# Kernel tuning notes

Measured on AMD Instinct MI355X. Metric: run time of the kernel, lower is better.

Reference implementation:

```python
import jax, jax.numpy as jnp
import numpy as np
import math

H = 1024
HEADS = 32
S = 4096
B = 3
E = 8192
QA = 2049  # start of QA span; content sentences cover [1, 2049)


def setup_inputs() -> dict:
    key = jax.random.key(0)
    ks = jax.random.split(key, 12)
    hidden_states = jax.random.normal(ks[0], (B, S, H), dtype=jnp.float32)
    st_mask = jax.random.randint(ks[1], (B, S), 0, 2, dtype=jnp.int64)
    edges_src = jax.random.randint(ks[2], (E,), 0, S, dtype=jnp.int64)
    edges_tgt = jax.random.randint(ks[3], (E,), 0, S, dtype=jnp.int64)
    edges_type = jax.random.randint(ks[4], (E,), 0, 26, dtype=jnp.int64)
    edges_pos = jax.random.randint(ks[5], (E,), 0, S, dtype=jnp.int64)
    # 32 content sentences of length 64 covering [1, 2049), then the QA span (2049, 4096)
    begins = 1 + 64 * np.arange(32)
    ends = begins + 64
    pairs = np.stack([np.append(begins, QA), np.append(ends, S)], axis=1).reshape(-1)
    all_sen = np.tile(pairs, (B, 1)).astype(np.int64)  # kept as numpy: static span indices
    scale = 0.02
    Wq = jax.random.normal(ks[6], (H, H), jnp.float32) * scale
    Wk = jax.random.normal(ks[7], (H, H), jnp.float32) * scale
    Wv = jax.random.normal(ks[8], (H, H), jnp.float32) * scale
    Wo = jax.random.normal(ks[9], (H, H), jnp.float32) * scale
    bq = jnp.zeros((H,), jnp.float32)
    bk = jnp.zeros((H,), jnp.float32)
    bv = jnp.zeros((H,), jnp.float32)
    bo = jnp.zeros((H,), jnp.float32)
    return dict(hidden_states=hidden_states, st_mask=st_mask, edges_src=edges_src,
                edges_tgt=edges_tgt, edges_type=edges_type, edges_pos=edges_pos,
                all_sen=all_sen, Wq=Wq, bq=bq, Wk=Wk, bk=bk, Wv=Wv, bv=bv, Wo=Wo, bo=bo)


def reference(hidden_states, st_mask, edges_src, edges_tgt, edges_type, edges_pos,
              all_sen, Wq, bq, Wk, bk, Wv, bv, Wo, bo):
    h = HEADS
    d_model = hidden_states.shape[-1]
    dk = d_model // h
    inv_sqrt_dk = 1.0 / math.sqrt(dk)

    def mha(q, k, v):
        # q: [Lq, H]; k, v: [Lk, H] -> [Lq, H]  (dropout is identity in eval mode)
        q2 = (q @ Wq.T + bq).reshape(-1, h, dk).transpose(1, 0, 2)  # [h, Lq, dk]
        k2 = (k @ Wk.T + bk).reshape(-1, h, dk).transpose(1, 0, 2)  # [h, Lk, dk]
        v2 = (v @ Wv.T + bv).reshape(-1, h, dk).transpose(1, 0, 2)
        scores = jnp.einsum('hqd,hkd->hqk', q2, k2) * inv_sqrt_dk
        p = jax.nn.softmax(scores, axis=-1)
        x = jnp.einsum('hqk,hkd->hqd', p, v2).transpose(1, 0, 2).reshape(-1, d_model)
        return x @ Wo.T + bo

    sen = np.asarray(all_sen)  # static span indices (host constants)
    outs = []
    for i in range(hidden_states.shape[0]):  # fixed small batch of 3
        pairs = sen[i][sen[i] != -1].reshape(-1, 2)
        qa, end = int(pairs[-1, 0]), int(pairs[-1, 1])
        q = hidden_states[i, 1:qa]       # [qa-1, H]
        kv = hidden_states[i, qa:end]    # [end-qa, H]
        hq1q2 = mha(q, kv, kv)           # content attends to QA span
        hq2q1 = mha(kv, q, q)            # QA span attends to content
        # hidden_states2 analogue: zeros elsewhere, attended reps in the two spans
        row = jnp.zeros_like(hidden_states[i])
        row = row.at[1:qa].set(hq1q2).at[qa:end].set(hq2q1)
        # per-sentence means (hidden_states3)
        sent_means = jnp.stack([row[b:e].mean(axis=0) for b, e in pairs])  # [n_sen, H]
        V11 = sent_means[:-1].mean(axis=0)  # mean over content-sentence means
        V21 = sent_means[-1]                # QA-span mean
        outs.append(jnp.concatenate([V11, V21]))
    return jnp.stack(outs)  # [3, 2H]
```

## Files before the change

### kernel.cpp

```cpp
#include <hip/hip_runtime.h>
#include <cstddef>

typedef __attribute__((ext_vector_type(8))) short bf16x8;
typedef __attribute__((ext_vector_type(4))) float f32x4;
typedef __attribute__((ext_vector_type(4))) unsigned short u16x4;
typedef __attribute__((ext_vector_type(8))) unsigned short u16x8;

namespace {
constexpr int B_ = 3, S_ = 4096, H_ = 1024, NH_ = 32;
constexpr int SEG1 = 1, SEG2 = 2049;
constexpr int NQ1 = 2048, NK1 = 2047, NQ2 = 2047, NK2 = 2048;
constexpr float SCALE = 0.17677669529663687f;
constexpr float LOG2E = 1.4426950408889634f;
constexpr float QSC   = SCALE * LOG2E;

constexpr size_t oXb = 0;
constexpr size_t oWb = oXb + (size_t)12288 * 1024 * 2;
constexpr size_t oBB = oWb + (size_t)2048 * 1024 * 2;
constexpr size_t oQH = oBB + (size_t)2048 * 4;
constexpr size_t oKH = oQH + (size_t)6 * 32 * 2048 * 32 * 2;
constexpr size_t oNL = oKH + (size_t)6 * 32 * 2048 * 32 * 2;
constexpr size_t oCS = oNL + (size_t)6 * 2048 * 4;
constexpr size_t oU  = oCS + (size_t)6 * 32 * 2048 * 4;
constexpr size_t oMv = oU  + (size_t)6 * 32 * 1024 * 4;
constexpr size_t oUP = oMv + (size_t)6 * 1024 * 4;
}

#if __has_builtin(__builtin_amdgcn_exp2f)
#define EXP2(x) __builtin_amdgcn_exp2f(x)
#else
#define EXP2(x) exp2f(x)
#endif
#if __has_builtin(__builtin_amdgcn_logf)
#define LOG2(x) __builtin_amdgcn_logf(x)
#else
#define LOG2(x) log2f(x)
#endif

__device__ __forceinline__ unsigned short f2bf(float f) {
    unsigned u = __float_as_uint(f);
    u += 0x7FFF + ((u >> 16) & 1);
    return (unsigned short)(u >> 16);
}
__device__ __forceinline__ float bf2f(unsigned short u) {
    return __uint_as_float((unsigned)u << 16);
}
__device__ __forceinline__ void gl16(const unsigned short* gp, unsigned short* lp) {
    __builtin_amdgcn_global_load_lds(
        (const __attribute__((address_space(1))) unsigned int*)gp,
        (__attribute__((address_space(3))) unsigned int*)lp, 16, 0, 0);
}

__global__ __launch_bounds__(256) void conv_x(const float* __restrict__ X,
                                              unsigned short* __restrict__ Xb)
{
    const size_t i4 = (size_t)blockIdx.x * 256 + threadIdx.x;
    const float4 v = *(const float4*)&X[i4 * 4];
    u16x4 o;
    o[0] = f2bf(v.x); o[1] = f2bf(v.y); o[2] = f2bf(v.z); o[3] = f2bf(v.w);
    *(u16x4*)&Xb[i4 * 4] = o;
}

__global__ __launch_bounds__(256) void conv_w(const float* __restrict__ Wq,
                                              const float* __restrict__ bq,
                                              const float* __restrict__ Wk,
                                              const float* __restrict__ bk,
                                              unsigned short* __restrict__ Wb,
                                              float* __restrict__ bb,
                                              unsigned short* __restrict__ QH,
                                              unsigned short* __restrict__ KH)
{
    const int i4 = blockIdx.x * 256 + threadIdx.x;
    const int base = i4 * 4;
    const bool isQ = base < (1 << 20);
    const float sc = isQ ? QSC : 1.f;
    const float* src = isQ ? &Wq[base] : &Wk[base - (1 << 20)];
    const float4 v = *(const float4*)src;
    u16x4 o;
    o[0] = f2bf(v.x * sc); o[1] = f2bf(v.y * sc);
    o[2] = f2bf(v.z * sc); o[3] = f2bf(v.w * sc);
    *(u16x4*)&Wb[base] = o;
    if (base < 2048) {
#pragma unroll
        for (int c = 0; c < 4; ++c) {
            const int j = base + c;
            bb[j] = (j < 1024) ? QSC * bq[j] : bk[j - 1024];
        }
    }
    if (i4 < 3072) {
        const int b = i4 >> 10, rem = i4 & 1023, h = rem >> 5, c = rem & 31;
        QH[(((size_t)(b * 2 + 1) * NH_ + h) * 2048 + 2047) * 32 + c] = 0;
        KH[(((size_t)(b * 2 + 0) * NH_ + h) * 2048 + 2047) * 32 + c] = 0;
    }
}

__global__ __launch_bounds__(256) void proj_mfma(const unsigned short* __restrict__ Xb,
                                                 const unsigned short* __restrict__ Wb,
                                                 const float* __restrict__ bb,
                                                 unsigned short* __restrict__ QH,
                                                 unsigned short* __restrict__ KH)
{
    __shared__ unsigned short ldsX[3 * 4096];
    __shared__ unsigned short ldsW[3 * 4096];
    const int tid = threadIdx.x;
    const int lane = tid & 63, w = tid >> 6;
    const int m0 = blockIdx.x * 128;
    const int n0 = blockIdx.y * 128;
    const int cr = (w >> 1) * 64;
    const int xc = (w & 1) * 64;

    const int co = ((lane & 3) ^ ((lane >> 3) & 3)) * 8;
    const unsigned short* gX = Xb + (size_t)(m0 + 32 * w + (lane >> 2)) * 1024 + co;
    const unsigned short* gW = Wb + (size_t)(n0 + 32 * w + (lane >> 2)) * 1024 + co;

#define STAGE(K0, BUF) do { \
    gl16(gX + (K0),             &ldsX[(BUF) * 4096 + (32 * w) * 32]); \
    gl16(gX + (K0) + 16 * 1024, &ldsX[(BUF) * 4096 + (32 * w + 16) * 32]); \
    gl16(gW + (K0),             &ldsW[(BUF) * 4096 + (32 * w) * 32]); \
    gl16(gW + (K0) + 16 * 1024, &ldsW[(BUF) * 4096 + (32 * w + 16) * 32]); \
} while (0)

    const int lr = lane & 15, lg = lane >> 4;
    const int mrW = cr + lr, mrX = xc + lr;
    const int oW = mrW * 32 + ((lg ^ ((mrW >> 1) & 3)) * 8);
    const int oX = mrX * 32 + ((lg ^ ((mrX >> 1) & 3)) * 8);

    f32x4 acc[4][4] = {};
    STAGE(0, 0);
    STAGE(32, 1);
    asm volatile("s_waitcnt vmcnt(4)" ::: "memory");
    __builtin_amdgcn_s_barrier();

    int cur = 0, stg = 2;
    for (int kt = 0; kt < 32; ++kt) {
        const int cb = cur * 4096;
        bf16x8 wf[4], xf[4];
#pragma unroll
        for (int i = 0; i < 4; ++i) wf[i] = *(const bf16x8*)&ldsW[cb + oW + i * 512];
#pragma unroll
        for (int j = 0; j < 4; ++j) xf[j] = *(const bf16x8*)&ldsX[cb + oX + j * 512];
        if (kt + 2 < 32) STAGE((kt + 2) * 32, stg);
#pragma unroll
        for (int i = 0; i < 4; ++i)
#pragma unroll
            for (int j = 0; j < 4; ++j)
                acc[i][j] = __builtin_amdgcn_mfma_f32_16x16x32_bf16(wf[i], xf[j], acc[i][j], 0, 0, 0);
        if (kt + 2 < 32) asm volatile("s_waitcnt vmcnt(4) lgkmcnt(0)" ::: "memory");
        else             asm volatile("s_waitcnt vmcnt(0) lgkmcnt(0)" ::: "memory");
        __builtin_amdgcn_s_barrier();
        cur = (cur == 2) ? 0 : cur + 1;
        stg = (stg == 2) ? 0 : stg + 1;
    }
#undef STAGE

    const bool sideK = (n0 >= 1024);
    unsigned short* dst = sideK ? KH : QH;

    int rowoff[4];
#pragma unroll
    for (int j = 0; j < 4; ++j) {
        const int g = m0 + xc + 16 * j + lr;
        const int b = g >> 12, rr = g & 4095;
        int v = -1;
        if (rr >= 2049) {
            const int seg = b * 2 + (sideK ? 0 : 1);
            v = seg * (NH_ * 2048 * 32) + (rr - 2049) * 32;
        } else if (rr >= 1) {
            const int seg = b * 2 + (sideK ? 1 : 0);
            v = seg * (NH_ * 2048 * 32) + (rr - 1) * 32;
        }
        rowoff[j] = v;
    }

    int coloff[4]; f32x4 bias4[4];
#pragma unroll
    for (int i = 0; i < 4; ++i) {
        const int c = n0 + cr + 16 * i + lg * 4;
        const int local = c - (sideK ? 1024 : 0);
        coloff[i] = (local >> 5) * (2048 * 32) + (local & 31);
        bias4[i] = *(const f32x4*)&bb[c];
    }

#pragma unroll
    for (int j = 0; j < 4; ++j) {
        if (rowoff[j] < 0) continue;
#pragma unroll
        for (int i = 0; i < 4; ++i) {
            u16x4 o;
#pragma unroll
            for (int r = 0; r < 4; ++r) o[r] = f2bf(acc[i][j][r] + bias4[i][r]);
            *(u16x4*)&dst[(size_t)rowoff[j] + coloff[i]] = o;
        }
    }
}

__global__ __launch_bounds__(256) void zpass(const unsigned short* __restrict__ QH,
                                             const unsigned short* __restrict__ KH,
                                             float* __restrict__ NL)
{
    const int tid = threadIdx.x, lane = tid & 63, w = tid >> 6;
    const int pan = blockIdx.x;
    const int bm = pan >> 5, mha = bm & 1;
    const int nq = mha ? NQ2 : NQ1, nk = mha ? NK2 : NK1;
    const size_t panel = (size_t)pan * 2048 * 32;
    const int lr = lane & 15, lg = lane >> 4;
    const int q0 = blockIdx.y * 256 + w * 64;
    const f32x4 zero = {0.f, 0.f, 0.f, 0.f};

    const unsigned short* Qp = QH + panel + (size_t)(q0 + lr) * 32 + lg * 8;
    const unsigned short* Kp = KH + panel + (size_t)lr * 32 + lg * 8;

    bf16x8 a[4];
#pragma unroll
    for (int i = 0; i < 4; ++i) a[i] = *(const bf16x8*)(Qp + i * 16 * 32);

    bf16x8 kb0 = *(const bf16x8*)(Kp);
    bf16x8 kb1 = *(const bf16x8*)(Kp + 512);

    f32x4 z[4] = {zero, zero, zero, zero};
    for (int kt = 0; kt < 126; kt += 2) {
        const bf16x8 n0 = *(const bf16x8*)(Kp + (size_t)(kt + 2) * 512);
        const bf16x8 n1 = *(const bf16x8*)(Kp + (size_t)(kt + 3) * 512);
#pragma unroll
        for (int i = 0; i < 4; ++i) {
            const f32x4 d = __builtin_amdgcn_mfma_f32_16x16x32_bf16(a[i], kb0, zero, 0, 0, 0);
            f32x4 e;
#pragma unroll
            for (int r = 0; r < 4; ++r) e[r] = EXP2(d[r]);
            z[i] += e;
        }
#pragma unroll
        for (int i = 0; i < 4; ++i) {
            const f32x4 d = __builtin_amdgcn_mfma_f32_16x16x32_bf16(a[i], kb1, zero, 0, 0, 0);
            f32x4 e;
#pragma unroll
            for (int r = 0; r < 4; ++r) e[r] = EXP2(d[r]);
            z[i] += e;
        }
        kb0 = n0; kb1 = n1;
    }
#pragma unroll
    for (int i = 0; i < 4; ++i) {
        const f32x4 d = __builtin_amdgcn_mfma_f32_16x16x32_bf16(a[i], kb0, zero, 0, 0, 0);
        f32x4 e;
#pragma unroll
        for (int r = 0; r < 4; ++r) e[r] = EXP2(d[r]);
        z[i] += e;
    }
    {
        const float m = (2032 + lr < nk) ? 1.f : 0.f;
#pragma unroll
        for (int i = 0; i < 4; ++i) {
            const f32x4 d = __builtin_amdgcn_mfma_f32_16x16x32_bf16(a[i], kb1, zero, 0, 0, 0);
            f32x4 e;
#pragma unroll
            for (int r = 0; r < 4; ++r) e[r] = m * EXP2(d[r]);
            z[i] += e;
        }
    }

#pragma unroll
    for (int i = 0; i < 4; ++i) {
        f32x4 zi = z[i];
#pragma unroll
        for (int r = 0; r < 4; ++r) {
            float v = zi[r];
            v += __shfl_xor(v, 1, 64);
            v += __shfl_xor(v, 2, 64);
            v += __shfl_xor(v, 4, 64);
            v += __shfl_xor(v, 8, 64);
            zi[r] = v;
        }
        if (lr == 0) {
            const int qb = q0 + i * 16 + lg * 4;
            f32x4 o;
#pragma unroll
            for (int r = 0; r < 4; ++r)
                o[r] = (qb + r < nq) ? -LOG2(zi[r]) : -1e30f;
            *(f32x4*)&NL[(size_t)bm * 2048 + qb] = o;
        }
    }
}

__global__ __launch_bounds__(256) void colsum(const unsigned short* __restrict__ QH,
                                              const unsigned short* __restrict__ KH,
                                              const float* __restrict__ NL,
                                              float* __restrict__ CS)
{
    const int tid = threadIdx.x, lane = tid & 63, w = tid >> 6;
    const int pan = blockIdx.x;
    const int bm = pan >> 5, mha = bm & 1;
    const int nk = mha ? NK2 : NK1;
    const size_t panel = (size_t)pan * 2048 * 32;
    const int lr = lane & 15, lg = lane >> 4;
    const int kc = blockIdx.y * 256 + w * 64;
    const f32x4 zero = {0.f, 0.f, 0.f, 0.f};

    const unsigned short* Kp = KH + panel + (size_t)(kc + lr) * 32 + lg * 8;
    const unsigned short* Qp = QH + panel + (size_t)lr * 32 + lg * 8;
    const float* zp = NL + (size_t)bm * 2048 + lg * 4;

    bf16x8 kb[4];
#pragma unroll
    for (int j = 0; j < 4; ++j) kb[j] = *(const bf16x8*)(Kp + j * 16 * 32);

    bf16x8 ai0 = *(const bf16x8*)(Qp);
    f32x4  cv0 = *(const f32x4*)(zp);
    bf16x8 ai1 = *(const bf16x8*)(Qp + 512);
    f32x4  cv1 = *(const f32x4*)(zp + 16);

    f32x4 cacc[4] = {zero, zero, zero, zero};
    for (int qt = 0; qt < 126; qt += 2) {
        const bf16x8 an0 = *(const bf16x8*)(Qp + (size_t)(qt + 2) * 512);
        const f32x4  cn0 = *(const f32x4*)(zp + (qt + 2) * 16);
        const bf16x8 an1 = *(const bf16x8*)(Qp + (size_t)(qt + 3) * 512);
        const f32x4  cn1 = *(const f32x4*)(zp + (qt + 3) * 16);
#pragma unroll
        for (int j = 0; j < 4; ++j) {
            const f32x4 d = __builtin_amdgcn_mfma_f32_16x16x32_bf16(ai0, kb[j], cv0, 0, 0, 0);
            f32x4 e;
#pragma unroll
            for (int r = 0; r < 4; ++r) e[r] = EXP2(d[r]);
            cacc[j] += e;
        }
#pragma unroll
        for (int j = 0; j < 4; ++j) {
            const f32x4 d = __builtin_amdgcn_mfma_f32_16x16x32_bf16(ai1, kb[j], cv1, 0, 0, 0);
            f32x4 e;
#pragma unroll
            for (int r = 0; r < 4; ++r) e[r] = EXP2(d[r]);
            cacc[j] += e;
        }
        ai0 = an0; cv0 = cn0; ai1 = an1; cv1 = cn1;
    }
#pragma unroll
    for (int j = 0; j < 4; ++j) {
        const f32x4 d = __builtin_amdgcn_mfma_f32_16x16x32_bf16(ai0, kb[j], cv0, 0, 0, 0);
        f32x4 e;
#pragma unroll
        for (int r = 0; r < 4; ++r) e[r] = EXP2(d[r]);
        cacc[j] += e;
    }
#pragma unroll
    for (int j = 0; j < 4; ++j) {
        const f32x4 d = __builtin_amdgcn_mfma_f32_16x16x32_bf16(ai1, kb[j], cv1, 0, 0, 0);
        f32x4 e;
#pragma unroll
        for (int r = 0; r < 4; ++r) e[r] = EXP2(d[r]);
        cacc[j] += e;
    }

#pragma unroll
    for (int j = 0; j < 4; ++j) {
        float v = (cacc[j][0] + cacc[j][1]) + (cacc[j][2] + cacc[j][3]);
        v += __shfl_xor(v, 16, 64);
        v += __shfl_xor(v, 32, 64);
        const int col = kc + 16 * j + lr;
        if (lane < 16 && col < nk)
            CS[(size_t)pan * 2048 + col] = v;
    }
}

__global__ __launch_bounds__(256) void colsum_x(
    const unsigned short* __restrict__ Xb, const float* __restrict__ CS,
    float* __restrict__ UP)
{
    __shared__ float sl[8][128];
    const int tid = threadIdx.x;
    const int bm = blockIdx.z;
    const int b = bm >> 1, mha = bm & 1;
    const int kbase = mha ? SEG1 : SEG2;
    const int nk = mha ? NK2 : NK1;
    const int kt = blockIdx.x;
    const int k0 = kt * 128;
    const int hg = blockIdx.y * 8;

    for (int idx = tid; idx < 8 * 128; idx += 256) {
        const int hh = idx >> 7, kk = idx & 127;
        const int k = k0 + kk;
        sl[hh][kk] = (k < nk) ? CS[((size_t)bm * NH_ + hg + hh) * 2048 + k] : 0.f;
    }
    __syncthreads();

    float acc[8][4] = {};
    const int c4 = tid * 4;
#pragma unroll 4
    for (int kk = 0; kk < 128; ++kk) {
        const int k = k0 + kk;
        const int krow = (k < nk) ? k : 0;
        const u16x4 xv = *(const u16x4*)&Xb[((size_t)b * S_ + kbase + krow) * H_ + c4];
        const float x0 = bf2f(xv[0]), x1 = bf2f(xv[1]), x2 = bf2f(xv[2]), x3 = bf2f(xv[3]);
#pragma unroll
        for (int hh = 0; hh < 8; ++hh) {
            const float sv = sl[hh][kk];
            acc[hh][0] += sv * x0; acc[hh][1] += sv * x1;
            acc[hh][2] += sv * x2; acc[hh][3] += sv * x3;
        }
    }
#pragma unroll
    for (int hh = 0; hh < 8; ++hh) {
        f32x4 o; o[0] = acc[hh][0]; o[1] = acc[hh][1]; o[2] = acc[hh][2]; o[3] = acc[hh][3];
        *(f32x4*)&UP[((size_t)(bm * NH_ + hg + hh) * 16 + kt) * 1024 + c4] = o;
    }
}

__global__ __launch_bounds__(256) void reduce_u(const float* __restrict__ UP,
                                                float* __restrict__ U)
{
    const int gid = blockIdx.x * 256 + threadIdx.x;
    const int row = gid >> 8;
    const int c4 = (gid & 255) * 4;
    const float* p = UP + (size_t)row * 16 * 1024 + c4;
    f32x4 s = *(const f32x4*)p;
#pragma unroll
    for (int t = 1; t < 16; ++t) s += *(const f32x4*)(p + t * 1024);
    *(f32x4*)&U[(size_t)row * 1024 + c4] = s;
}

__global__ __launch_bounds__(256) void compute_m(
    const float* __restrict__ U, const float* __restrict__ Wv,
    const float* __restrict__ bv, float* __restrict__ Mvec)
{
    const int bm = blockIdx.y;
    const int mha = bm & 1;
    const float invnq = 1.f / (float)(mha ? NQ2 : NQ1);
    const int o = blockIdx.x * 256 + threadIdx.x;
    const int hh = o >> 5;
    const float* u = &U[((size_t)bm * NH_ + hh) * H_];
    const float* w = &Wv[(size_t)o * H_];
    float acc = 0.f;
    for (int in = 0; in < H_; in += 4) {
        const float4 uv = *(const float4*)&u[in];
        const float4 wv = *(const float4*)&w[in];
        acc += uv.x * wv.x + uv.y * wv.y + uv.z * wv.z + uv.w * wv.w;
    }
    Mvec[(size_t)bm * H_ + o] = acc * invnq + bv[o];
}

__global__ __launch_bounds__(256) void final_out(
    const float* __restrict__ Mvec, const float* __restrict__ Wo,
    const float* __restrict__ bo, float* __restrict__ out)
{
    const int bm = blockIdx.y;
    const int b = bm >> 1, mha = bm & 1;
    const int o = blockIdx.x * 256 + threadIdx.x;
    const float* mv = &Mvec[(size_t)bm * H_];
    const float* w = &Wo[(size_t)o * H_];
    float acc = 0.f;
    for (int in = 0; in < H_; in += 4) {
        const float4 mvv = *(const float4*)&mv[in];
        const float4 wv = *(const float4*)&w[in];
        acc += mvv.x * wv.x + mvv.y * wv.y + mvv.z * wv.z + mvv.w * wv.w;
    }
    out[(size_t)b * 2048 + mha * 1024 + o] = acc + bo[o];
}

extern "C" void kernel_launch(void* const* d_in, const int* in_sizes, int n_in,
                              void* d_out, int out_size, void* d_ws, size_t ws_size,
                              hipStream_t stream)
{
    const float* hidden = (const float*)d_in[0];
    const float* Wq = (const float*)d_in[7];
    const float* bq = (const float*)d_in[8];
    const float* Wk = (const float*)d_in[9];
    const float* bk = (const float*)d_in[10];
    const float* Wv = (const float*)d_in[11];
    const float* bv = (const float*)d_in[12];
    const float* Wo = (const float*)d_in[13];
    const float* bo = (const float*)d_in[14];
    float* out = (float*)d_out;
    char* ws = (char*)d_ws;

    unsigned short* Xb  = (unsigned short*)(ws + oXb);
    unsigned short* Wb  = (unsigned short*)(ws + oWb);
    float* bb           = (float*)(ws + oBB);
    unsigned short* QHp = (unsigned short*)(ws + oQH);
    unsigned short* KHp = (unsigned short*)(ws + oKH);
    float* NL           = (float*)(ws + oNL);
    float* CS           = (float*)(ws + oCS);
    float* U            = (float*)(ws + oU);
    float* Mv           = (float*)(ws + oMv);
    float* UP           = (float*)(ws + oUP);

    const dim3 blk(256);
    conv_x<<<12288, blk, 0, stream>>>(hidden, Xb);
    conv_w<<<2048, blk, 0, stream>>>(Wq, bq, Wk, bk, Wb, bb, QHp, KHp);
    proj_mfma<<<dim3(96, 16), blk, 0, stream>>>(Xb, Wb, bb, QHp, KHp);
    zpass<<<dim3(192, 8), blk, 0, stream>>>(QHp, KHp, NL);
    colsum<<<dim3(192, 8), blk, 0, stream>>>(QHp, KHp, NL, CS);
    colsum_x<<<dim3(16, 4, 6), blk, 0, stream>>>(Xb, CS, UP);
    reduce_u<<<192, blk, 0, stream>>>(UP, U);
    compute_m<<<dim3(4, 6), blk, 0, stream>>>(U, Wv, bv, Mv);
    final_out<<<dim3(4, 6), blk, 0, stream>>>(Mv, Wo, bo, out);
}
```

Before: 377.2 us.

## Use K=64 double-buffered LDS tiles with 8-way swizzle in projection GEMM

The projection GEMM moves from a triple-buffered K=32 LDS pipeline to a double-buffered K=64 one. Each iteration now runs two MFMA sub-steps, and the XOR swizzle is widened to 8 chunks to fit 64-column rows. The goal is to halve the number of barriers and loop iterations and to issue larger global-to-LDS loads per stage. In exchange, prefetch depth drops from two stages ahead to one, and every iteration waits on vmcnt(0), so load latency may be less well hidden. LDS use grows from 48 KB to 64 KB per block, which could lower occupancy.

```diff
diff --git a/kernel.cpp b/kernel.cpp
--- a/kernel.cpp
+++ b/kernel.cpp
@@ -100,8 +100,8 @@
                                                  unsigned short* __restrict__ QH,
                                                  unsigned short* __restrict__ KH)
 {
-    __shared__ unsigned short ldsX[3 * 4096];
-    __shared__ unsigned short ldsW[3 * 4096];
+    __shared__ unsigned short ldsX[2][8192];
+    __shared__ unsigned short ldsW[2][8192];
     const int tid = threadIdx.x;
     const int lane = tid & 63, w = tid >> 6;
     const int m0 = blockIdx.x * 128;
@@ -109,47 +109,64 @@
     const int cr = (w >> 1) * 64;
     const int xc = (w & 1) * 64;
 
-    const int co = ((lane & 3) ^ ((lane >> 3) & 3)) * 8;
-    const unsigned short* gX = Xb + (size_t)(m0 + 32 * w + (lane >> 2)) * 1024 + co;
-    const unsigned short* gW = Wb + (size_t)(n0 + 32 * w + (lane >> 2)) * 1024 + co;
+    const int srow = 32 * w + (lane >> 3);
+    const int sco  = ((lane & 7) ^ (lane >> 3)) * 8;
+    const unsigned short* gX = Xb + (size_t)(m0 + srow) * 1024 + sco;
+    const unsigned short* gW = Wb + (size_t)(n0 + srow) * 1024 + sco;
 
 #define STAGE(K0, BUF) do { \
-    gl16(gX + (K0),             &ldsX[(BUF) * 4096 + (32 * w) * 32]); \
-    gl16(gX + (K0) + 16 * 1024, &ldsX[(BUF) * 4096 + (32 * w + 16) * 32]); \
-    gl16(gW + (K0),             &ldsW[(BUF) * 4096 + (32 * w) * 32]); \
-    gl16(gW + (K0) + 16 * 1024, &ldsW[(BUF) * 4096 + (32 * w + 16) * 32]); \
+    gl16(gX + (K0),             &ldsX[BUF][(32 * w +  0) * 64]); \
+    gl16(gX + (K0) +  8 * 1024, &ldsX[BUF][(32 * w +  8) * 64]); \
+    gl16(gX + (K0) + 16 * 1024, &ldsX[BUF][(32 * w + 16) * 64]); \
+    gl16(gX + (K0) + 24 * 1024, &ldsX[BUF][(32 * w + 24) * 64]); \
+    gl16(gW + (K0),             &ldsW[BUF][(32 * w +  0) * 64]); \
+    gl16(gW + (K0) +  8 * 1024, &ldsW[BUF][(32 * w +  8) * 64]); \
+    gl16(gW + (K0) + 16 * 1024, &ldsW[BUF][(32 * w + 16) * 64]); \
+    gl16(gW + (K0) + 24 * 1024, &ldsW[BUF][(32 * w + 24) * 64]); \
 } while (0)
 
     const int lr = lane & 15, lg = lane >> 4;
+    const int swz = lr & 7;
     const int mrW = cr + lr, mrX = xc + lr;
-    const int oW = mrW * 32 + ((lg ^ ((mrW >> 1) & 3)) * 8);
-    const int oX = mrX * 32 + ((lg ^ ((mrX >> 1) & 3)) * 8);
+    const int oW0 = mrW * 64 + ((lg ^ swz) * 8);
+    const int oW1 = mrW * 64 + (((4 + lg) ^ swz) * 8);
+    const int oX0 = mrX * 64 + ((lg ^ swz) * 8);
+    const int oX1 = mrX * 64 + (((4 + lg) ^ swz) * 8);
 
     f32x4 acc[4][4] = {};
     STAGE(0, 0);
-    STAGE(32, 1);
-    asm volatile("s_waitcnt vmcnt(4)" ::: "memory");
+    asm volatile("s_waitcnt vmcnt(0)" ::: "memory");
     __builtin_amdgcn_s_barrier();
 
-    int cur = 0, stg = 2;
-    for (int kt = 0; kt < 32; ++kt) {
-        const int cb = cur * 4096;
-        bf16x8 wf[4], xf[4];
-#pragma unroll
-        for (int i = 0; i < 4; ++i) wf[i] = *(const bf16x8*)&ldsW[cb + oW + i * 512];
-#pragma unroll
-        for (int j = 0; j < 4; ++j) xf[j] = *(const bf16x8*)&ldsX[cb + oX + j * 512];
-        if (kt + 2 < 32) STAGE((kt + 2) * 32, stg);
-#pragma unroll
-        for (int i = 0; i < 4; ++i)
-#pragma unroll
-            for (int j = 0; j < 4; ++j)
-                acc[i][j] = __builtin_amdgcn_mfma_f32_16x16x32_bf16(wf[i], xf[j], acc[i][j], 0, 0, 0);
-        if (kt + 2 < 32) asm volatile("s_waitcnt vmcnt(4) lgkmcnt(0)" ::: "memory");
-        else             asm volatile("s_waitcnt vmcnt(0) lgkmcnt(0)" ::: "memory");
+    for (int t = 0; t < 16; ++t) {
+        const int buf = t & 1;
+        if (t < 15) STAGE((t + 1) * 64, buf ^ 1);
+        {
+            bf16x8 wf[4], xf[4];
+#pragma unroll
+            for (int i = 0; i < 4; ++i) wf[i] = *(const bf16x8*)&ldsW[buf][oW0 + i * 1024];
+#pragma unroll
+            for (int j = 0; j < 4; ++j) xf[j] = *(const bf16x8*)&ldsX[buf][oX0 + j * 1024];
+#pragma unroll
+            for (int i = 0; i < 4; ++i)
+#pragma unroll
+                for (int j = 0; j < 4; ++j)
+                    acc[i][j] = __builtin_amdgcn_mfma_f32_16x16x32_bf16(wf[i], xf[j], acc[i][j], 0, 0, 0);
+        }
+        {
+            bf16x8 wf[4], xf[4];
+#pragma unroll
+            for (int i = 0; i < 4; ++i) wf[i] = *(const bf16x8*)&ldsW[buf][oW1 + i * 1024];
+#pragma unroll
+            for (int j = 0; j < 4; ++j) xf[j] = *(const bf16x8*)&ldsX[buf][oX1 + j * 1024];
+#pragma unroll
+            for (int i = 0; i < 4; ++i)
+#pragma unroll
+                for (int j = 0; j < 4; ++j)
+                    acc[i][j] = __builtin_amdgcn_mfma_f32_16x16x32_bf16(wf[i], xf[j], acc[i][j], 0, 0, 0);
+        }
+        asm volatile("s_waitcnt vmcnt(0) lgkmcnt(0)" ::: "memory");
         __builtin_amdgcn_s_barrier();
-        cur = (cur == 2) ? 0 : cur + 1;
-        stg = (stg == 2) ? 0 : stg + 1;
     }
 #undef STAGE
 
```

Result: slower. 389.7 us (median of 2 runs) (+3.3%).
